# Kernel optimization log

Measured on AMD Instinct MI355X. Metric: run time of the kernel, lower is better.

Reference implementation:

```python
import jax, jax.numpy as jnp
import numpy as np

B, S, D, H = 4, 2048, 768, 12
DH = D // H  # depth per head = 64


def setup_inputs() -> dict:
    key = jax.random.key(0)
    ks = jax.random.split(key, 10)
    s = 0.02
    return {
        "layer_input": jax.random.normal(ks[0], (B, S, D), jnp.float32),
        "mask": jnp.zeros((B, 1, 1, S), jnp.float32),
        "wq": jax.random.normal(ks[1], (D, D), jnp.float32) * s,
        "bq": jnp.zeros((D,), jnp.float32),
        "wk": jax.random.normal(ks[2], (D, D), jnp.float32) * s,
        "bk": jnp.zeros((D,), jnp.float32),
        "wv": jax.random.normal(ks[3], (D, D), jnp.float32) * s,
        "bv": jnp.zeros((D,), jnp.float32),
        "wo": jax.random.normal(ks[4], (D, D), jnp.float32) * s,
        "bo": jnp.zeros((D,), jnp.float32),
    }


def _split_heads(x):
    # [B, S, D] -> [B, H, S, DH]
    b, s, _ = x.shape
    return x.reshape(b, s, H, DH).transpose(0, 2, 1, 3)


def reference(layer_input, mask, wq, bq, wk, bk, wv, bv, wo, bo):
    q = _split_heads(layer_input @ wq + bq)
    k = _split_heads(layer_input @ wk + bk)
    v = _split_heads(layer_input @ wv + bv)
    # scaled dot-product attention; scores [B, H, S, S]
    logits = jnp.einsum("bhqd,bhkd->bhqk", q, k) / jnp.sqrt(jnp.float32(DH))
    logits = logits + mask * (-1e9)
    attn = jax.nn.softmax(logits, axis=-1)
    ctx = jnp.einsum("bhqk,bhkd->bhqd", attn, v)  # [B, H, S, DH]
    concat = ctx.transpose(0, 2, 1, 3).reshape(layer_input.shape[0], -1, D)
    return concat @ wo + bo
```

## Files before the change

kernel.cpp:

```cpp
#include <hip/hip_runtime.h>
#include <hip/hip_bf16.h>

#define NB 4
#define NS 2048
#define ND 768
#define NH 12
#define NDH 64
#define NM (NB * NS)

#define QSCALE 0.1803368867f
#define MSCALE (-1.442695041e9f)

typedef __attribute__((ext_vector_type(8))) short short8;
typedef __attribute__((ext_vector_type(4))) float f32x4;
typedef __attribute__((ext_vector_type(16))) float f32x16;

__device__ __forceinline__ void async_ld16(const void* g, void* l) {
  __builtin_amdgcn_global_load_lds(
      (const __attribute__((address_space(1))) void*)g,
      (__attribute__((address_space(3))) void*)l, 16, 0, 0);
}

__device__ __forceinline__ unsigned pack_bf16(float a, float b) {
  return ((unsigned)__bfloat16_as_ushort(__float2bfloat16(b)) << 16) |
         (unsigned)__bfloat16_as_ushort(__float2bfloat16(a));
}

__device__ __forceinline__ void permlane_swap(unsigned& a, unsigned& b) {
  asm("v_permlane32_swap_b32 %0, %1" : "+v"(a), "+v"(b));
}

__device__ __forceinline__ float fast_exp2(float x) {
  float r;
  asm("v_exp_f32 %0, %1" : "=v"(r) : "v"(x));
  return r;
}

__global__ __launch_bounds__(256) void convert_bf16_kernel(
    const float* __restrict__ in, __hip_bfloat16* __restrict__ out, int n8) {
  const int i = blockIdx.x * 256 + threadIdx.x;
  if (i >= n8) return;
  const float4 a = ((const float4*)in)[i * 2];
  const float4 b = ((const float4*)in)[i * 2 + 1];
  short8 v;
  __hip_bfloat16* p = (__hip_bfloat16*)&v;
  p[0] = __float2bfloat16(a.x); p[1] = __float2bfloat16(a.y);
  p[2] = __float2bfloat16(a.z); p[3] = __float2bfloat16(a.w);
  p[4] = __float2bfloat16(b.x); p[5] = __float2bfloat16(b.y);
  p[6] = __float2bfloat16(b.z); p[7] = __float2bfloat16(b.w);
  ((short8*)out)[i] = v;
}

__global__ __launch_bounds__(256) void mask_perm_kernel(
    const float* __restrict__ mask, float* __restrict__ mperm_g,
    unsigned* __restrict__ mbits) {
  const int idx = blockIdx.x * 256 + threadIdx.x;
  const int b = idx >> 11;
  const int sb = idx & 2047;
  const int tile = sb >> 6, slot = sb & 63;
  const int g = slot >> 5, hh = (slot >> 4) & 1, r = slot & 15;
  const int key = tile * 64 + g * 32 + 4 * hh + (r & 3) + 8 * (r >> 2);
  const float v = mask[b * NS + key];
  mperm_g[idx] = v * MSCALE;
  if (v != 0.f) atomicOr(&mbits[b], 1u << tile);
}

__global__ __launch_bounds__(256) void transpose_w_kernel(
    const float* __restrict__ w0, const float* __restrict__ w1,
    const float* __restrict__ w2, const float* __restrict__ w3,
    __hip_bfloat16* __restrict__ WtAll) {
  __shared__ __hip_bfloat16 tile[64][66];
  const float* src = blockIdx.z == 0 ? w0 : blockIdx.z == 1 ? w1
                   : blockIdx.z == 2 ? w2 : w3;
  __hip_bfloat16* dst = WtAll + (size_t)blockIdx.z * ND * ND;
  const int kk0 = blockIdx.y * 64, nn0 = blockIdx.x * 64;
  const int t = threadIdx.x;
#pragma unroll
  for (int p = 0; p < 4; ++p) {
    const int idx = p * 256 + t;
    const int k = idx >> 4;
    const int c = (idx & 15) * 4;
    const float4 v = *(const float4*)(src + (size_t)(kk0 + k) * ND + nn0 + c);
    __hip_bfloat162* tp = (__hip_bfloat162*)&tile[k][c];
    tp[0] = __hip_bfloat162{__float2bfloat16(v.x), __float2bfloat16(v.y)};
    tp[1] = __hip_bfloat162{__float2bfloat16(v.z), __float2bfloat16(v.w)};
  }
  __syncthreads();
#pragma unroll
  for (int p = 0; p < 2; ++p) {
    const int idx = p * 256 + t;
    const int n = idx >> 3;
    const int kb = (idx & 7) * 8;
    short8 v;
    __hip_bfloat16* pv = (__hip_bfloat16*)&v;
#pragma unroll
    for (int j = 0; j < 8; ++j) pv[j] = tile[kb + j][n];
    *(short8*)(dst + (size_t)(nn0 + n) * ND + kk0 + kb) = v;
  }
}

__global__ __launch_bounds__(256) void qkv_gemm_kernel(
    const __hip_bfloat16* __restrict__ A,
    const __hip_bfloat16* __restrict__ Bt,
    const float* __restrict__ bq, const float* __restrict__ bk,
    const float* __restrict__ bv,
    __hip_bfloat16* __restrict__ Qw, __hip_bfloat16* __restrict__ Kw,
    __hip_bfloat16* __restrict__ Vt) {
  __shared__ __hip_bfloat16 As[128 * 32];
  __shared__ __hip_bfloat16 Bs[128 * 32];
  const int K = ND;
  const int tid = threadIdx.x;
  const int w = tid >> 6, l = tid & 63;
  const int lk = l & 15, lt = l >> 4;
  const int p = blockIdx.x + 18 * blockIdx.y;
  const int swzb = (p & 7) * 144 + (p >> 3);
  const int m0 = (swzb / 18) * 128, n0 = (swzb % 18) * 128;
  const int wr = w >> 1, wc = w & 1;

  f32x4 acc[4][4] = {};

  const int arow = w * 32 + (l >> 2);
  const int acol = (l & 3) * 8;
  const __hip_bfloat16* aptr = A + (size_t)(m0 + arow) * K + acol;
  const __hip_bfloat16* bptr = Bt + (size_t)(n0 + arow) * K + acol;
  __hip_bfloat16* asb = As + w * 1024;
  __hip_bfloat16* bsb = Bs + w * 1024;

  for (int k0 = 0; k0 < K; k0 += 32) {
    __syncthreads();
    async_ld16(aptr + k0, asb);
    async_ld16(aptr + (size_t)16 * K + k0, asb + 512);
    async_ld16(bptr + k0, bsb);
    async_ld16(bptr + (size_t)16 * K + k0, bsb + 512);
    __syncthreads();

    short8 af[4], bf[4];
#pragma unroll
    for (int m = 0; m < 4; ++m)
      af[m] = *(const short8*)(As + (wr * 64 + m * 16 + lk) * 32 + lt * 8);
#pragma unroll
    for (int n = 0; n < 4; ++n)
      bf[n] = *(const short8*)(Bs + (wc * 64 + n * 16 + lk) * 32 + lt * 8);
#pragma unroll
    for (int m = 0; m < 4; ++m)
#pragma unroll
      for (int n = 0; n < 4; ++n)
        acc[m][n] =
            __builtin_amdgcn_mfma_f32_16x16x32_bf16(af[m], bf[n], acc[m][n], 0, 0, 0);
  }

  const int mi = n0 / ND;
  const int nbase = n0 - mi * ND;
  const float* bp = mi == 0 ? bq : mi == 1 ? bk : bv;
  const float oscale = (mi == 0) ? QSCALE : 1.f;

#pragma unroll
  for (int n = 0; n < 4; ++n) {
    const int col = nbase + wc * 64 + n * 16 + lk;
    const float bb = bp[col];
#pragma unroll
    for (int m = 0; m < 4; ++m) {
      const int row = m0 + wr * 64 + m * 16 + lt * 4;
#pragma unroll
      for (int r = 0; r < 4; ++r) {
        const float v = (acc[m][n][r] + bb) * oscale;
        if (mi < 2) {
          (mi ? Kw : Qw)[(size_t)(row + r) * ND + col] = __float2bfloat16(v);
        } else {
          const int mrow = row + r;
          const int bidx = mrow >> 11, s = mrow & 2047;
          const int hh = col >> 6, dh = col & 63;
          Vt[(((size_t)bidx * NH + hh) * NDH + dh) * NS + s] = __float2bfloat16(v);
        }
      }
    }
  }
}

__global__ __launch_bounds__(256) void mha_mfma32_kernel(
    const __hip_bfloat16* __restrict__ Qb, const __hip_bfloat16* __restrict__ Kb,
    const __hip_bfloat16* __restrict__ Vt, const float* __restrict__ mperm_g,
    const unsigned* __restrict__ maskbits, __hip_bfloat16* __restrict__ ctx) {
  __shared__ __align__(16) char smem[32768];
  char* KsB = smem;
  char* VsB = smem + 16384;

  const int p = blockIdx.x + 16 * (blockIdx.y + 12 * blockIdx.z);
  const int logical = (p & 7) * 96 + (p >> 3);
  const int lx = logical & 15;
  const int rest = logical >> 4;
  const int h = rest % 12;
  const int b = rest / 12;

  const int tid = threadIdx.x;
  const int w = tid >> 6, l = tid & 63;
  const int l31 = l & 31, hi = l >> 5;
  const int q0 = lx * 128 + w * 32;
  const unsigned mbitsb = maskbits[b];

  const __hip_bfloat16* qp = Qb + ((size_t)b * NS + q0 + l31) * ND + h * NDH;
  short8 qf[4];
#pragma unroll
  for (int ks = 0; ks < 4; ++ks)
    qf[ks] = *(const short8*)(qp + ks * 16 + hi * 8);

  const short ONEB = 0x3F80;
  const short8 ones = {ONEB, ONEB, ONEB, ONEB, ONEB, ONEB, ONEB, ONEB};

  f32x16 c0 = {}, c1 = {}, lacc = {};
  const f32x16 z16 = {};

  const int srow = l >> 3, slot = l & 7;
  const int key1 = w * 8 + srow, key2 = key1 + 32;
  const __hip_bfloat16* kg1 =
      Kb + ((size_t)b * NS + key1) * ND + h * NDH + (slot ^ (key1 & 7)) * 8;
  const __hip_bfloat16* kg2 =
      Kb + ((size_t)b * NS + key2) * ND + h * NDH + (slot ^ (key2 & 7)) * 8;
  const __hip_bfloat16* vg1 =
      Vt + (((size_t)b * NH + h) * NDH + key1) * NS + (slot ^ (key1 & 7)) * 8;
  const __hip_bfloat16* vg2 =
      Vt + (((size_t)b * NH + h) * NDH + key2) * NS + (slot ^ (key2 & 7)) * 8;
  const int ldsoff = w * 1024;
  const float* mg = mperm_g + (size_t)b * NS;

#define STAGE(buf, t)                                                        \
  {                                                                          \
    const size_t koff = (size_t)(t) * 64 * ND;                               \
    char* kd = KsB + (buf) * 8192 + ldsoff;                                  \
    char* vd = VsB + (buf) * 8192 + ldsoff;                                  \
    async_ld16(kg1 + koff, kd);                                              \
    async_ld16(kg2 + koff, kd + 4096);                                       \
    async_ld16(vg1 + (t) * 64, vd);                                          \
    async_ld16(vg2 + (t) * 64, vd + 4096);                                   \
  }

  const int swz = (l31 & 7) << 4;

  auto compute_tile = [&](int t, int cur2) {
    const int bufo = cur2 * 8192;
    f32x16 s0, s1;
#pragma unroll
    for (int ks = 0; ks < 4; ++ks) {
      const int off = (((ks << 5) | (hi << 4)) ^ swz);
      const short8 kf0 = *(const short8*)(KsB + bufo + (l31 << 7) + off);
      const short8 kf1 = *(const short8*)(KsB + bufo + ((32 + l31) << 7) + off);
      if (ks == 0) {
        s0 = __builtin_amdgcn_mfma_f32_32x32x16_bf16(kf0, qf[0], z16, 0, 0, 0);
        s1 = __builtin_amdgcn_mfma_f32_32x32x16_bf16(kf1, qf[0], z16, 0, 0, 0);
      } else {
        s0 = __builtin_amdgcn_mfma_f32_32x32x16_bf16(kf0, qf[ks], s0, 0, 0, 0);
        s1 = __builtin_amdgcn_mfma_f32_32x32x16_bf16(kf1, qf[ks], s1, 0, 0, 0);
      }
    }

    if ((mbitsb >> t) & 1) {
      const float* mgt = mg + t * 64 + hi * 16;
#pragma unroll
      for (int r = 0; r < 16; ++r) {
        s0[r] += mgt[r];
        s1[r] += mgt[32 + r];
      }
    }

#pragma unroll
    for (int r = 0; r < 16; ++r) s0[r] = fast_exp2(s0[r]);
#pragma unroll
    for (int r = 0; r < 16; ++r) s1[r] = fast_exp2(s1[r]);

#pragma unroll
    for (int ks = 0; ks < 4; ++ks) {
      const f32x16& S = (ks < 2) ? s0 : s1;
      const int r0 = (ks & 1) * 8;
      unsigned u0 = pack_bf16(S[r0 + 0], S[r0 + 1]);
      unsigned u1 = pack_bf16(S[r0 + 2], S[r0 + 3]);
      unsigned u2 = pack_bf16(S[r0 + 4], S[r0 + 5]);
      unsigned u3 = pack_bf16(S[r0 + 6], S[r0 + 7]);
      permlane_swap(u0, u2);
      permlane_swap(u1, u3);
      union { unsigned u[4]; short8 v; } pf = {{u0, u1, u2, u3}};
      const int off = (((ks << 5) | (hi << 4)) ^ swz);
      const short8 vf0 = *(const short8*)(VsB + bufo + (l31 << 7) + off);
      c0 = __builtin_amdgcn_mfma_f32_32x32x16_bf16(vf0, pf.v, c0, 0, 0, 0);
      const short8 vf1 = *(const short8*)(VsB + bufo + ((32 + l31) << 7) + off);
      c1 = __builtin_amdgcn_mfma_f32_32x32x16_bf16(vf1, pf.v, c1, 0, 0, 0);
      lacc = __builtin_amdgcn_mfma_f32_32x32x16_bf16(ones, pf.v, lacc, 0, 0, 0);
    }
  };

  STAGE(0, 0);
  for (int t = 0; t < 32; ++t) {
    asm volatile("s_waitcnt vmcnt(0) lgkmcnt(0)" ::: "memory");
    __builtin_amdgcn_s_barrier();
    if (t + 1 < 32) STAGE((t + 1) & 1, t + 1);
    compute_tile(t, t & 1);
  }

  const float inv = 1.f / lacc[0];

  __syncthreads();
  __hip_bfloat16* cb = (__hip_bfloat16*)(smem + w * 4864);
#pragma unroll
  for (int mg2 = 0; mg2 < 2; ++mg2) {
    const f32x16& cc = mg2 ? c1 : c0;
#pragma unroll
    for (int rr = 0; rr < 4; ++rr) {
      const unsigned u0 = pack_bf16(cc[rr * 4 + 0] * inv, cc[rr * 4 + 1] * inv);
      const unsigned u1 = pack_bf16(cc[rr * 4 + 2] * inv, cc[rr * 4 + 3] * inv);
      *(uint2*)(cb + l31 * 76 + mg2 * 32 + 4 * hi + 8 * rr) = uint2{u0, u1};
    }
  }
  __syncthreads();
  const __hip_bfloat16* crd =
      (const __hip_bfloat16*)(smem + w * 4864) + (l >> 1) * 76 + (l & 1) * 8;
  __hip_bfloat16* gout =
      ctx + ((size_t)b * NS + q0 + (l >> 1)) * ND + h * NDH + (l & 1) * 8;
#pragma unroll
  for (int i = 0; i < 4; ++i) {
    const uint2 a = *(const uint2*)(crd + i * 16);
    const uint2 b2 = *(const uint2*)(crd + i * 16 + 4);
    *(uint4*)(gout + i * 16) = uint4{a.x, a.y, b2.x, b2.y};
  }
#undef STAGE
}

__global__ __launch_bounds__(256) void gemm_bt_mfma_kernel(
    const __hip_bfloat16* __restrict__ A, const __hip_bfloat16* __restrict__ Bt,
    const float* __restrict__ bias, float* __restrict__ Cout,
    int M, int N, int K) {
  __shared__ __hip_bfloat16 As[128 * 32];
  __shared__ __hip_bfloat16 Bs[64 * 32];
  const int tid = threadIdx.x;
  const int w = tid >> 6, l = tid & 63;
  const int lk = l & 15, lt = l >> 4;
  const int p = blockIdx.x + 12 * blockIdx.y;
  const int swzb = (p & 7) * 96 + (p >> 3);
  const int m0 = (swzb / 12) * 128, n0 = (swzb % 12) * 64;
  const int wr = w >> 1, wc = w & 1;

  f32x4 acc[4][2] = {};

  const int arow = w * 32 + (l >> 2);
  const int acol = (l & 3) * 8;
  const __hip_bfloat16* aptr = A + (size_t)(m0 + arow) * K + acol;
  const int brow = w * 16 + (l >> 2);
  const __hip_bfloat16* bptr = Bt + (size_t)(n0 + brow) * K + acol;
  __hip_bfloat16* asb = As + w * 1024;
  __hip_bfloat16* bsb = Bs + w * 512;

  for (int k0 = 0; k0 < K; k0 += 32) {
    __syncthreads();
    async_ld16(aptr + k0, asb);
    async_ld16(aptr + (size_t)16 * K + k0, asb + 512);
    async_ld16(bptr + k0, bsb);
    __syncthreads();

    short8 af[4], bf[2];
#pragma unroll
    for (int m = 0; m < 4; ++m)
      af[m] = *(const short8*)(As + (wr * 64 + m * 16 + lk) * 32 + lt * 8);
#pragma unroll
    for (int n = 0; n < 2; ++n)
      bf[n] = *(const short8*)(Bs + (wc * 32 + n * 16 + lk) * 32 + lt * 8);
#pragma unroll
    for (int m = 0; m < 4; ++m)
#pragma unroll
      for (int n = 0; n < 2; ++n)
        acc[m][n] =
            __builtin_amdgcn_mfma_f32_16x16x32_bf16(af[m], bf[n], acc[m][n], 0, 0, 0);
  }

#pragma unroll
  for (int n = 0; n < 2; ++n) {
    const int col = n0 + wc * 32 + n * 16 + lk;
    const float bb = bias[col];
#pragma unroll
    for (int m = 0; m < 4; ++m) {
      const int row = m0 + wr * 64 + m * 16 + lt * 4;
#pragma unroll
      for (int r = 0; r < 4; ++r)
        Cout[(size_t)(row + r) * N + col] = acc[m][n][r] + bb;
    }
  }
}

extern "C" void kernel_launch(void* const* d_in, const int* in_sizes, int n_in,
                              void* d_out, int out_size, void* d_ws, size_t ws_size,
                              hipStream_t stream) {
  const float* x    = (const float*)d_in[0];
  const float* mask = (const float*)d_in[1];
  const float* wq   = (const float*)d_in[2];
  const float* bq   = (const float*)d_in[3];
  const float* wk   = (const float*)d_in[4];
  const float* bk   = (const float*)d_in[5];
  const float* wv   = (const float*)d_in[6];
  const float* bv   = (const float*)d_in[7];
  const float* wo   = (const float*)d_in[8];
  const float* bo   = (const float*)d_in[9];
  float* out = (float*)d_out;

  const size_t mat = (size_t)NM * ND;
  const size_t wmat = (size_t)ND * ND;
  __hip_bfloat16* xb    = (__hip_bfloat16*)d_ws;
  __hip_bfloat16* WtAll = xb + mat;
  __hip_bfloat16* Qw    = WtAll + 4 * wmat;
  __hip_bfloat16* Kw    = Qw + mat;
  __hip_bfloat16* Vtw   = Kw + mat;
  __hip_bfloat16* Cw    = Vtw + mat;
  float* mpg            = (float*)(Cw + mat);
  unsigned* mbits       = (unsigned*)(mpg + NM);

  convert_bf16_kernel<<<(NM * ND / 8 + 255) / 256, 256, 0, stream>>>(
      x, xb, NM * ND / 8);
  hipMemsetAsync(mbits, 0, NB * sizeof(unsigned), stream);
  mask_perm_kernel<<<NM / 256, 256, 0, stream>>>(mask, mpg, mbits);
  transpose_w_kernel<<<dim3(ND / 64, ND / 64, 4), 256, 0, stream>>>(
      wq, wk, wv, wo, WtAll);

  qkv_gemm_kernel<<<dim3(3 * ND / 128, NM / 128), 256, 0, stream>>>(
      xb, WtAll, bq, bk, bv, Qw, Kw, Vtw);

  mha_mfma32_kernel<<<dim3(NS / 128, NH, NB), 256, 0, stream>>>(
      Qw, Kw, Vtw, mpg, mbits, Cw);

  gemm_bt_mfma_kernel<<<dim3(ND / 64, NM / 128), 256, 0, stream>>>(
      Cw, WtAll + 3 * wmat, bo, out, NM, ND, ND);
}
```

Before: 176.6 us.

## Process 64 queries per wave in attention, halving block to two waves

```diff
diff --git a/kernel.cpp b/kernel.cpp
--- a/kernel.cpp
+++ b/kernel.cpp
@@ -177,7 +177,7 @@
   }
 }
 
-__global__ __launch_bounds__(256) void mha_mfma32_kernel(
+__global__ __launch_bounds__(128) void mha_mfma32_kernel(
     const __hip_bfloat16* __restrict__ Qb, const __hip_bfloat16* __restrict__ Kb,
     const __hip_bfloat16* __restrict__ Vt, const float* __restrict__ mperm_g,
     const unsigned* __restrict__ maskbits, __hip_bfloat16* __restrict__ ctx) {
@@ -195,95 +195,164 @@
   const int tid = threadIdx.x;
   const int w = tid >> 6, l = tid & 63;
   const int l31 = l & 31, hi = l >> 5;
-  const int q0 = lx * 128 + w * 32;
+  const int q0 = lx * 128 + w * 64;
   const unsigned mbitsb = maskbits[b];
 
-  const __hip_bfloat16* qp = Qb + ((size_t)b * NS + q0 + l31) * ND + h * NDH;
-  short8 qf[4];
-#pragma unroll
-  for (int ks = 0; ks < 4; ++ks)
-    qf[ks] = *(const short8*)(qp + ks * 16 + hi * 8);
+  const __hip_bfloat16* qpA = Qb + ((size_t)b * NS + q0 + l31) * ND + h * NDH;
+  const __hip_bfloat16* qpB = qpA + 32 * ND;
+  short8 qfA[4], qfB[4];
+#pragma unroll
+  for (int ks = 0; ks < 4; ++ks) {
+    qfA[ks] = *(const short8*)(qpA + ks * 16 + hi * 8);
+    qfB[ks] = *(const short8*)(qpB + ks * 16 + hi * 8);
+  }
 
   const short ONEB = 0x3F80;
   const short8 ones = {ONEB, ONEB, ONEB, ONEB, ONEB, ONEB, ONEB, ONEB};
 
-  f32x16 c0 = {}, c1 = {}, lacc = {};
+  f32x16 cA0 = {}, cA1 = {}, cB0 = {}, cB1 = {}, lA = {}, lB = {};
   const f32x16 z16 = {};
 
-  const int srow = l >> 3, slot = l & 7;
-  const int key1 = w * 8 + srow, key2 = key1 + 32;
-  const __hip_bfloat16* kg1 =
-      Kb + ((size_t)b * NS + key1) * ND + h * NDH + (slot ^ (key1 & 7)) * 8;
-  const __hip_bfloat16* kg2 =
-      Kb + ((size_t)b * NS + key2) * ND + h * NDH + (slot ^ (key2 & 7)) * 8;
-  const __hip_bfloat16* vg1 =
-      Vt + (((size_t)b * NH + h) * NDH + key1) * NS + (slot ^ (key1 & 7)) * 8;
-  const __hip_bfloat16* vg2 =
-      Vt + (((size_t)b * NH + h) * NDH + key2) * NS + (slot ^ (key2 & 7)) * 8;
-  const int ldsoff = w * 1024;
+  const int srow = w * 32 + (l >> 3);
+  const int colswz = ((l & 7) ^ (l >> 3)) * 8;
+  const __hip_bfloat16* kg =
+      Kb + ((size_t)b * NS + srow) * ND + h * NDH + colswz;
+  const __hip_bfloat16* vg =
+      Vt + (((size_t)b * NH + h) * NDH + srow) * NS + colswz;
   const float* mg = mperm_g + (size_t)b * NS;
 
 #define STAGE(buf, t)                                                        \
   {                                                                          \
+    char* kd = KsB + (buf) * 8192 + w * 4096;                                \
+    char* vd = VsB + (buf) * 8192 + w * 4096;                                \
     const size_t koff = (size_t)(t) * 64 * ND;                               \
-    char* kd = KsB + (buf) * 8192 + ldsoff;                                  \
-    char* vd = VsB + (buf) * 8192 + ldsoff;                                  \
-    async_ld16(kg1 + koff, kd);                                              \
-    async_ld16(kg2 + koff, kd + 4096);                                       \
-    async_ld16(vg1 + (t) * 64, vd);                                          \
-    async_ld16(vg2 + (t) * 64, vd + 4096);                                   \
+    async_ld16(kg + koff, kd);                                               \
+    async_ld16(kg + koff + (size_t)8 * ND, kd + 1024);                       \
+    async_ld16(kg + koff + (size_t)16 * ND, kd + 2048);                      \
+    async_ld16(kg + koff + (size_t)24 * ND, kd + 3072);                      \
+    async_ld16(vg + (t) * 64, vd);                                           \
+    async_ld16(vg + (t) * 64 + 8 * NS, vd + 1024);                           \
+    async_ld16(vg + (t) * 64 + 16 * NS, vd + 2048);                          \
+    async_ld16(vg + (t) * 64 + 24 * NS, vd + 3072);                          \
   }
 
   const int swz = (l31 & 7) << 4;
 
   auto compute_tile = [&](int t, int cur2) {
     const int bufo = cur2 * 8192;
-    f32x16 s0, s1;
-#pragma unroll
-    for (int ks = 0; ks < 4; ++ks) {
-      const int off = (((ks << 5) | (hi << 4)) ^ swz);
-      const short8 kf0 = *(const short8*)(KsB + bufo + (l31 << 7) + off);
-      const short8 kf1 = *(const short8*)(KsB + bufo + ((32 + l31) << 7) + off);
-      if (ks == 0) {
-        s0 = __builtin_amdgcn_mfma_f32_32x32x16_bf16(kf0, qf[0], z16, 0, 0, 0);
-        s1 = __builtin_amdgcn_mfma_f32_32x32x16_bf16(kf1, qf[0], z16, 0, 0, 0);
-      } else {
-        s0 = __builtin_amdgcn_mfma_f32_32x32x16_bf16(kf0, qf[ks], s0, 0, 0, 0);
-        s1 = __builtin_amdgcn_mfma_f32_32x32x16_bf16(kf1, qf[ks], s1, 0, 0, 0);
+    const float* mgt = mg + t * 64 + hi * 16;
+    const bool hasmask = (mbitsb >> t) & 1;
+
+    {
+      f32x16 sA, sB;
+      const int ro = bufo + (l31 << 7);
+#pragma unroll
+      for (int ks = 0; ks < 4; ++ks) {
+        const short8 kf =
+            *(const short8*)(KsB + ro + (((ks << 5) | (hi << 4)) ^ swz));
+        if (ks == 0) {
+          sA = __builtin_amdgcn_mfma_f32_32x32x16_bf16(kf, qfA[0], z16, 0, 0, 0);
+          sB = __builtin_amdgcn_mfma_f32_32x32x16_bf16(kf, qfB[0], z16, 0, 0, 0);
+        } else {
+          sA = __builtin_amdgcn_mfma_f32_32x32x16_bf16(kf, qfA[ks], sA, 0, 0, 0);
+          sB = __builtin_amdgcn_mfma_f32_32x32x16_bf16(kf, qfB[ks], sB, 0, 0, 0);
+        }
+      }
+      if (hasmask) {
+#pragma unroll
+        for (int r = 0; r < 16; ++r) {
+          sA[r] += mgt[r];
+          sB[r] += mgt[r];
+        }
+      }
+#pragma unroll
+      for (int r = 0; r < 16; ++r) sA[r] = fast_exp2(sA[r]);
+#pragma unroll
+      for (int r = 0; r < 16; ++r) sB[r] = fast_exp2(sB[r]);
+
+#pragma unroll
+      for (int ss = 0; ss < 2; ++ss) {
+        const int r0 = ss * 8;
+        unsigned a0 = pack_bf16(sA[r0 + 0], sA[r0 + 1]);
+        unsigned a1 = pack_bf16(sA[r0 + 2], sA[r0 + 3]);
+        unsigned a2 = pack_bf16(sA[r0 + 4], sA[r0 + 5]);
+        unsigned a3 = pack_bf16(sA[r0 + 6], sA[r0 + 7]);
+        permlane_swap(a0, a2);
+        permlane_swap(a1, a3);
+        union { unsigned u[4]; short8 v; } pfA = {{a0, a1, a2, a3}};
+        unsigned b0 = pack_bf16(sB[r0 + 0], sB[r0 + 1]);
+        unsigned b1 = pack_bf16(sB[r0 + 2], sB[r0 + 3]);
+        unsigned b2 = pack_bf16(sB[r0 + 4], sB[r0 + 5]);
+        unsigned b3 = pack_bf16(sB[r0 + 6], sB[r0 + 7]);
+        permlane_swap(b0, b2);
+        permlane_swap(b1, b3);
+        union { unsigned u[4]; short8 v; } pfB = {{b0, b1, b2, b3}};
+        const int off = bufo + (((ss << 5) | (hi << 4)) ^ swz);
+        const short8 vf0 = *(const short8*)(VsB + off + (l31 << 7));
+        const short8 vf1 = *(const short8*)(VsB + off + ((32 + l31) << 7));
+        cA0 = __builtin_amdgcn_mfma_f32_32x32x16_bf16(vf0, pfA.v, cA0, 0, 0, 0);
+        cA1 = __builtin_amdgcn_mfma_f32_32x32x16_bf16(vf1, pfA.v, cA1, 0, 0, 0);
+        cB0 = __builtin_amdgcn_mfma_f32_32x32x16_bf16(vf0, pfB.v, cB0, 0, 0, 0);
+        cB1 = __builtin_amdgcn_mfma_f32_32x32x16_bf16(vf1, pfB.v, cB1, 0, 0, 0);
+        lA = __builtin_amdgcn_mfma_f32_32x32x16_bf16(ones, pfA.v, lA, 0, 0, 0);
+        lB = __builtin_amdgcn_mfma_f32_32x32x16_bf16(ones, pfB.v, lB, 0, 0, 0);
       }
     }
 
-    if ((mbitsb >> t) & 1) {
-      const float* mgt = mg + t * 64 + hi * 16;
-#pragma unroll
-      for (int r = 0; r < 16; ++r) {
-        s0[r] += mgt[r];
-        s1[r] += mgt[32 + r];
-      }
-    }
-
-#pragma unroll
-    for (int r = 0; r < 16; ++r) s0[r] = fast_exp2(s0[r]);
-#pragma unroll
-    for (int r = 0; r < 16; ++r) s1[r] = fast_exp2(s1[r]);
-
-#pragma unroll
-    for (int ks = 0; ks < 4; ++ks) {
-      const f32x16& S = (ks < 2) ? s0 : s1;
-      const int r0 = (ks & 1) * 8;
-      unsigned u0 = pack_bf16(S[r0 + 0], S[r0 + 1]);
-      unsigned u1 = pack_bf16(S[r0 + 2], S[r0 + 3]);
-      unsigned u2 = pack_bf16(S[r0 + 4], S[r0 + 5]);
-      unsigned u3 = pack_bf16(S[r0 + 6], S[r0 + 7]);
-      permlane_swap(u0, u2);
-      permlane_swap(u1, u3);
-      union { unsigned u[4]; short8 v; } pf = {{u0, u1, u2, u3}};
-      const int off = (((ks << 5) | (hi << 4)) ^ swz);
-      const short8 vf0 = *(const short8*)(VsB + bufo + (l31 << 7) + off);
-      c0 = __builtin_amdgcn_mfma_f32_32x32x16_bf16(vf0, pf.v, c0, 0, 0, 0);
-      const short8 vf1 = *(const short8*)(VsB + bufo + ((32 + l31) << 7) + off);
-      c1 = __builtin_amdgcn_mfma_f32_32x32x16_bf16(vf1, pf.v, c1, 0, 0, 0);
-      lacc = __builtin_amdgcn_mfma_f32_32x32x16_bf16(ones, pf.v, lacc, 0, 0, 0);
+    {
+      f32x16 sA, sB;
+      const int ro = bufo + ((32 + l31) << 7);
+#pragma unroll
+      for (int ks = 0; ks < 4; ++ks) {
+        const short8 kf =
+            *(const short8*)(KsB + ro + (((ks << 5) | (hi << 4)) ^ swz));
+        if (ks == 0) {
+          sA = __builtin_amdgcn_mfma_f32_32x32x16_bf16(kf, qfA[0], z16, 0, 0, 0);
+          sB = __builtin_amdgcn_mfma_f32_32x32x16_bf16(kf, qfB[0], z16, 0, 0, 0);
+        } else {
+          sA = __builtin_amdgcn_mfma_f32_32x32x16_bf16(kf, qfA[ks], sA, 0, 0, 0);
+          sB = __builtin_amdgcn_mfma_f32_32x32x16_bf16(kf, qfB[ks], sB, 0, 0, 0);
+        }
+      }
+      if (hasmask) {
+#pragma unroll
+        for (int r = 0; r < 16; ++r) {
+          sA[r] += mgt[32 + r];
+          sB[r] += mgt[32 + r];
+        }
+      }
+#pragma unroll
+      for (int r = 0; r < 16; ++r) sA[r] = fast_exp2(sA[r]);
+#pragma unroll
+      for (int r = 0; r < 16; ++r) sB[r] = fast_exp2(sB[r]);
+
+#pragma unroll
+      for (int ss = 2; ss < 4; ++ss) {
+        const int r0 = (ss - 2) * 8;
+        unsigned a0 = pack_bf16(sA[r0 + 0], sA[r0 + 1]);
+        unsigned a1 = pack_bf16(sA[r0 + 2], sA[r0 + 3]);
+        unsigned a2 = pack_bf16(sA[r0 + 4], sA[r0 + 5]);
+        unsigned a3 = pack_bf16(sA[r0 + 6], sA[r0 + 7]);
+        permlane_swap(a0, a2);
+        permlane_swap(a1, a3);
+        union { unsigned u[4]; short8 v; } pfA = {{a0, a1, a2, a3}};
+        unsigned b0 = pack_bf16(sB[r0 + 0], sB[r0 + 1]);
+        unsigned b1 = pack_bf16(sB[r0 + 2], sB[r0 + 3]);
+        unsigned b2 = pack_bf16(sB[r0 + 4], sB[r0 + 5]);
+        unsigned b3 = pack_bf16(sB[r0 + 6], sB[r0 + 7]);
+        permlane_swap(b0, b2);
+        permlane_swap(b1, b3);
+        union { unsigned u[4]; short8 v; } pfB = {{b0, b1, b2, b3}};
+        const int off = bufo + (((ss << 5) | (hi << 4)) ^ swz);
+        const short8 vf0 = *(const short8*)(VsB + off + (l31 << 7));
+        const short8 vf1 = *(const short8*)(VsB + off + ((32 + l31) << 7));
+        cA0 = __builtin_amdgcn_mfma_f32_32x32x16_bf16(vf0, pfA.v, cA0, 0, 0, 0);
+        cA1 = __builtin_amdgcn_mfma_f32_32x32x16_bf16(vf1, pfA.v, cA1, 0, 0, 0);
+        cB0 = __builtin_amdgcn_mfma_f32_32x32x16_bf16(vf0, pfB.v, cB0, 0, 0, 0);
+        cB1 = __builtin_amdgcn_mfma_f32_32x32x16_bf16(vf1, pfB.v, cB1, 0, 0, 0);
+        lA = __builtin_amdgcn_mfma_f32_32x32x16_bf16(ones, pfA.v, lA, 0, 0, 0);
+        lB = __builtin_amdgcn_mfma_f32_32x32x16_bf16(ones, pfB.v, lB, 0, 0, 0);
+      }
     }
   };
 
@@ -295,30 +364,35 @@
     compute_tile(t, t & 1);
   }
 
-  const float inv = 1.f / lacc[0];
+  const float invA = 1.f / lA[0];
+  const float invB = 1.f / lB[0];
 
   __syncthreads();
-  __hip_bfloat16* cb = (__hip_bfloat16*)(smem + w * 4864);
+  __hip_bfloat16* cb = (__hip_bfloat16*)(smem + w * 9728);
 #pragma unroll
   for (int mg2 = 0; mg2 < 2; ++mg2) {
-    const f32x16& cc = mg2 ? c1 : c0;
+    const f32x16& ca = mg2 ? cA1 : cA0;
+    const f32x16& cbv = mg2 ? cB1 : cB0;
 #pragma unroll
     for (int rr = 0; rr < 4; ++rr) {
-      const unsigned u0 = pack_bf16(cc[rr * 4 + 0] * inv, cc[rr * 4 + 1] * inv);
-      const unsigned u1 = pack_bf16(cc[rr * 4 + 2] * inv, cc[rr * 4 + 3] * inv);
-      *(uint2*)(cb + l31 * 76 + mg2 * 32 + 4 * hi + 8 * rr) = uint2{u0, u1};
+      const unsigned a0 = pack_bf16(ca[rr * 4 + 0] * invA, ca[rr * 4 + 1] * invA);
+      const unsigned a1 = pack_bf16(ca[rr * 4 + 2] * invA, ca[rr * 4 + 3] * invA);
+      *(uint2*)(cb + l31 * 76 + mg2 * 32 + 4 * hi + 8 * rr) = uint2{a0, a1};
+      const unsigned b0 = pack_bf16(cbv[rr * 4 + 0] * invB, cbv[rr * 4 + 1] * invB);
+      const unsigned b1 = pack_bf16(cbv[rr * 4 + 2] * invB, cbv[rr * 4 + 3] * invB);
+      *(uint2*)(cb + (32 + l31) * 76 + mg2 * 32 + 4 * hi + 8 * rr) = uint2{b0, b1};
     }
   }
   __syncthreads();
-  const __hip_bfloat16* crd =
-      (const __hip_bfloat16*)(smem + w * 4864) + (l >> 1) * 76 + (l & 1) * 8;
-  __hip_bfloat16* gout =
-      ctx + ((size_t)b * NS + q0 + (l >> 1)) * ND + h * NDH + (l & 1) * 8;
-#pragma unroll
-  for (int i = 0; i < 4; ++i) {
-    const uint2 a = *(const uint2*)(crd + i * 16);
-    const uint2 b2 = *(const uint2*)(crd + i * 16 + 4);
-    *(uint4*)(gout + i * 16) = uint4{a.x, a.y, b2.x, b2.y};
+#pragma unroll
+  for (int i = 0; i < 8; ++i) {
+    const int row = i * 8 + (l >> 3);
+    const __hip_bfloat16* crd = cb + row * 76 + (l & 7) * 8;
+    const uint2 a = *(const uint2*)(crd);
+    const uint2 b2 = *(const uint2*)(crd + 4);
+    __hip_bfloat16* gout =
+        ctx + ((size_t)b * NS + q0 + row) * ND + h * NDH + (l & 7) * 8;
+    *(uint4*)(gout) = uint4{a.x, a.y, b2.x, b2.y};
   }
 #undef STAGE
 }
@@ -419,7 +493,7 @@
   qkv_gemm_kernel<<<dim3(3 * ND / 128, NM / 128), 256, 0, stream>>>(
       xb, WtAll, bq, bk, bv, Qw, Kw, Vtw);
 
-  mha_mfma32_kernel<<<dim3(NS / 128, NH, NB), 256, 0, stream>>>(
+  mha_mfma32_kernel<<<dim3(NS / 128, NH, NB), 128, 0, stream>>>(
       Qw, Kw, Vtw, mpg, mbits, Cw);
 
   gemm_bt_mfma_kernel<<<dim3(ND / 64, NM / 128), 256, 0, stream>>>(
```

After: 209.9 us. 18.8% more time.

## Fuse prep kernels into one launch and XOR-swizzle GEMM LDS tiles

Applied to the files above, without the earlier changes.

```diff
diff --git a/kernel.cpp b/kernel.cpp
--- a/kernel.cpp
+++ b/kernel.cpp
@@ -36,66 +36,78 @@
   return r;
 }
 
-__global__ __launch_bounds__(256) void convert_bf16_kernel(
-    const float* __restrict__ in, __hip_bfloat16* __restrict__ out, int n8) {
-  const int i = blockIdx.x * 256 + threadIdx.x;
-  if (i >= n8) return;
-  const float4 a = ((const float4*)in)[i * 2];
-  const float4 b = ((const float4*)in)[i * 2 + 1];
-  short8 v;
-  __hip_bfloat16* p = (__hip_bfloat16*)&v;
-  p[0] = __float2bfloat16(a.x); p[1] = __float2bfloat16(a.y);
-  p[2] = __float2bfloat16(a.z); p[3] = __float2bfloat16(a.w);
-  p[4] = __float2bfloat16(b.x); p[5] = __float2bfloat16(b.y);
-  p[6] = __float2bfloat16(b.z); p[7] = __float2bfloat16(b.w);
-  ((short8*)out)[i] = v;
-}
-
-__global__ __launch_bounds__(256) void mask_perm_kernel(
-    const float* __restrict__ mask, float* __restrict__ mperm_g,
-    unsigned* __restrict__ mbits) {
-  const int idx = blockIdx.x * 256 + threadIdx.x;
-  const int b = idx >> 11;
-  const int sb = idx & 2047;
-  const int tile = sb >> 6, slot = sb & 63;
-  const int g = slot >> 5, hh = (slot >> 4) & 1, r = slot & 15;
-  const int key = tile * 64 + g * 32 + 4 * hh + (r & 3) + 8 * (r >> 2);
-  const float v = mask[b * NS + key];
-  mperm_g[idx] = v * MSCALE;
-  if (v != 0.f) atomicOr(&mbits[b], 1u << tile);
-}
-
-__global__ __launch_bounds__(256) void transpose_w_kernel(
+__global__ __launch_bounds__(256) void prep_kernel(
+    const float* __restrict__ x, const float* __restrict__ mask,
     const float* __restrict__ w0, const float* __restrict__ w1,
     const float* __restrict__ w2, const float* __restrict__ w3,
-    __hip_bfloat16* __restrict__ WtAll) {
-  __shared__ __hip_bfloat16 tile[64][66];
-  const float* src = blockIdx.z == 0 ? w0 : blockIdx.z == 1 ? w1
-                   : blockIdx.z == 2 ? w2 : w3;
-  __hip_bfloat16* dst = WtAll + (size_t)blockIdx.z * ND * ND;
-  const int kk0 = blockIdx.y * 64, nn0 = blockIdx.x * 64;
+    __hip_bfloat16* __restrict__ xb, float* __restrict__ mperm_g,
+    unsigned* __restrict__ mbits, __hip_bfloat16* __restrict__ WtAll) {
+  __shared__ __align__(16) char pshm[8448];
+  const int bid = blockIdx.x;
   const int t = threadIdx.x;
-#pragma unroll
-  for (int p = 0; p < 4; ++p) {
-    const int idx = p * 256 + t;
-    const int k = idx >> 4;
-    const int c = (idx & 15) * 4;
-    const float4 v = *(const float4*)(src + (size_t)(kk0 + k) * ND + nn0 + c);
-    __hip_bfloat162* tp = (__hip_bfloat162*)&tile[k][c];
-    tp[0] = __hip_bfloat162{__float2bfloat16(v.x), __float2bfloat16(v.y)};
-    tp[1] = __hip_bfloat162{__float2bfloat16(v.z), __float2bfloat16(v.w)};
-  }
-  __syncthreads();
-#pragma unroll
-  for (int p = 0; p < 2; ++p) {
-    const int idx = p * 256 + t;
-    const int n = idx >> 3;
-    const int kb = (idx & 7) * 8;
+
+  if (bid < 3072) {
+    const int i = bid * 256 + t;
+    const float4 a = ((const float4*)x)[i * 2];
+    const float4 b = ((const float4*)x)[i * 2 + 1];
     short8 v;
-    __hip_bfloat16* pv = (__hip_bfloat16*)&v;
-#pragma unroll
-    for (int j = 0; j < 8; ++j) pv[j] = tile[kb + j][n];
-    *(short8*)(dst + (size_t)(nn0 + n) * ND + kk0 + kb) = v;
+    __hip_bfloat16* p = (__hip_bfloat16*)&v;
+    p[0] = __float2bfloat16(a.x); p[1] = __float2bfloat16(a.y);
+    p[2] = __float2bfloat16(a.z); p[3] = __float2bfloat16(a.w);
+    p[4] = __float2bfloat16(b.x); p[5] = __float2bfloat16(b.y);
+    p[6] = __float2bfloat16(b.z); p[7] = __float2bfloat16(b.w);
+    ((short8*)xb)[i] = v;
+  } else if (bid < 3648) {
+    auto tile = (__hip_bfloat16(*)[66])pshm;
+    const int tt = bid - 3072;
+    const int bz = tt / 144;
+    const int rem = tt % 144;
+    const int kk0 = (rem / 12) * 64, nn0 = (rem % 12) * 64;
+    const float* src = bz == 0 ? w0 : bz == 1 ? w1 : bz == 2 ? w2 : w3;
+    __hip_bfloat16* dst = WtAll + (size_t)bz * ND * ND;
+#pragma unroll
+    for (int pp = 0; pp < 4; ++pp) {
+      const int idx = pp * 256 + t;
+      const int k = idx >> 4;
+      const int c = (idx & 15) * 4;
+      const float4 v = *(const float4*)(src + (size_t)(kk0 + k) * ND + nn0 + c);
+      __hip_bfloat162* tp = (__hip_bfloat162*)&tile[k][c];
+      tp[0] = __hip_bfloat162{__float2bfloat16(v.x), __float2bfloat16(v.y)};
+      tp[1] = __hip_bfloat162{__float2bfloat16(v.z), __float2bfloat16(v.w)};
+    }
+    __syncthreads();
+#pragma unroll
+    for (int pp = 0; pp < 2; ++pp) {
+      const int idx = pp * 256 + t;
+      const int n = idx >> 3;
+      const int kb = (idx & 7) * 8;
+      short8 v;
+      __hip_bfloat16* pv = (__hip_bfloat16*)&v;
+#pragma unroll
+      for (int j = 0; j < 8; ++j) pv[j] = tile[kb + j][n];
+      *(short8*)(dst + (size_t)(nn0 + n) * ND + kk0 + kb) = v;
+    }
+  } else {
+    unsigned* red = (unsigned*)pshm;
+    const int b = bid - 3648;
+    unsigned mymask = 0;
+#pragma unroll
+    for (int j = 0; j < 8; ++j) {
+      const int sb = t * 8 + j;
+      const int tile = sb >> 6, slot = sb & 63;
+      const int g = slot >> 5, hh = (slot >> 4) & 1, r = slot & 15;
+      const int key = tile * 64 + g * 32 + 4 * hh + (r & 3) + 8 * (r >> 2);
+      const float v = mask[b * NS + key];
+      mperm_g[b * 2048 + sb] = v * MSCALE;
+      if (v != 0.f) mymask |= 1u << tile;
+    }
+    red[t] = mymask;
+    __syncthreads();
+    for (int s = 128; s > 0; s >>= 1) {
+      if (t < s) red[t] |= red[t + s];
+      __syncthreads();
+    }
+    if (t == 0) mbits[b] = red[0];
   }
 }
 
@@ -120,12 +132,14 @@
   f32x4 acc[4][4] = {};
 
   const int arow = w * 32 + (l >> 2);
-  const int acol = (l & 3) * 8;
+  const int acol = ((l & 3) ^ ((l >> 3) & 3)) * 8;
   const __hip_bfloat16* aptr = A + (size_t)(m0 + arow) * K + acol;
   const __hip_bfloat16* bptr = Bt + (size_t)(n0 + arow) * K + acol;
   __hip_bfloat16* asb = As + w * 1024;
   __hip_bfloat16* bsb = Bs + w * 1024;
 
+  const int sslot = (lt ^ ((lk >> 1) & 3)) << 3;
+
   for (int k0 = 0; k0 < K; k0 += 32) {
     __syncthreads();
     async_ld16(aptr + k0, asb);
@@ -137,10 +151,10 @@
     short8 af[4], bf[4];
 #pragma unroll
     for (int m = 0; m < 4; ++m)
-      af[m] = *(const short8*)(As + (wr * 64 + m * 16 + lk) * 32 + lt * 8);
+      af[m] = *(const short8*)(As + (wr * 64 + m * 16 + lk) * 32 + sslot);
 #pragma unroll
     for (int n = 0; n < 4; ++n)
-      bf[n] = *(const short8*)(Bs + (wc * 64 + n * 16 + lk) * 32 + lt * 8);
+      bf[n] = *(const short8*)(Bs + (wc * 64 + n * 16 + lk) * 32 + sslot);
 #pragma unroll
     for (int m = 0; m < 4; ++m)
 #pragma unroll
@@ -340,13 +354,15 @@
   f32x4 acc[4][2] = {};
 
   const int arow = w * 32 + (l >> 2);
-  const int acol = (l & 3) * 8;
+  const int acol = ((l & 3) ^ ((l >> 3) & 3)) * 8;
   const __hip_bfloat16* aptr = A + (size_t)(m0 + arow) * K + acol;
   const int brow = w * 16 + (l >> 2);
   const __hip_bfloat16* bptr = Bt + (size_t)(n0 + brow) * K + acol;
   __hip_bfloat16* asb = As + w * 1024;
   __hip_bfloat16* bsb = Bs + w * 512;
 
+  const int sslot = (lt ^ ((lk >> 1) & 3)) << 3;
+
   for (int k0 = 0; k0 < K; k0 += 32) {
     __syncthreads();
     async_ld16(aptr + k0, asb);
@@ -357,10 +373,10 @@
     short8 af[4], bf[2];
 #pragma unroll
     for (int m = 0; m < 4; ++m)
-      af[m] = *(const short8*)(As + (wr * 64 + m * 16 + lk) * 32 + lt * 8);
+      af[m] = *(const short8*)(As + (wr * 64 + m * 16 + lk) * 32 + sslot);
 #pragma unroll
     for (int n = 0; n < 2; ++n)
-      bf[n] = *(const short8*)(Bs + (wc * 32 + n * 16 + lk) * 32 + lt * 8);
+      bf[n] = *(const short8*)(Bs + (wc * 32 + n * 16 + lk) * 32 + sslot);
 #pragma unroll
     for (int m = 0; m < 4; ++m)
 #pragma unroll
@@ -409,12 +425,8 @@
   float* mpg            = (float*)(Cw + mat);
   unsigned* mbits       = (unsigned*)(mpg + NM);
 
-  convert_bf16_kernel<<<(NM * ND / 8 + 255) / 256, 256, 0, stream>>>(
-      x, xb, NM * ND / 8);
-  hipMemsetAsync(mbits, 0, NB * sizeof(unsigned), stream);
-  mask_perm_kernel<<<NM / 256, 256, 0, stream>>>(mask, mpg, mbits);
-  transpose_w_kernel<<<dim3(ND / 64, ND / 64, 4), 256, 0, stream>>>(
-      wq, wk, wv, wo, WtAll);
+  prep_kernel<<<3652, 256, 0, stream>>>(x, mask, wq, wk, wv, wo,
+                                        xb, mpg, mbits, WtAll);
 
   qkv_gemm_kernel<<<dim3(3 * ND / 128, NM / 128), 256, 0, stream>>>(
       xb, WtAll, bq, bk, bv, Qw, Kw, Vtw);
```

Result: faster. 171.2 us (-3.1%).
